# Performance work log

Hardware: AMD Instinct MI355X
Metric: run time of the kernel (lower is better)

Reference implementation:

```python
import jax, jax.numpy as jnp
import numpy as np

EPS = 1e-7  # K.epsilon()
ROUTINGS = 3

def squash(v, axis=-1):
    s2 = jnp.sum(jnp.square(v), axis=axis, keepdims=True)
    scale = s2 / (1.0 + s2) / jnp.sqrt(s2 + EPS)
    return scale * v

def setup_inputs() -> dict:
    key = jax.random.key(0)
    k1, k2 = jax.random.split(key)
    B, IN_CAPS, IN_DIM = 256, 1152, 8
    NUM_CAPS, DIM = 10, 16
    x = jax.random.normal(k1, (B, IN_CAPS, IN_DIM), dtype=jnp.float32)
    W = jax.random.normal(k2, (IN_CAPS, NUM_CAPS, IN_DIM, DIM), dtype=jnp.float32) * 0.05
    return {"x": x, "W": W}

def reference(x, W):
    # u_hat[b,i,j,d] = sum_k x[b,i,k] * W[i,j,k,d]
    u_hat = jnp.einsum('bik,ijkd->bijd', x, W)  # [B, in_caps, num_caps, dim]
    b = jnp.zeros(u_hat.shape[:-1], dtype=u_hat.dtype)  # [B, in_caps, num_caps]
    v = None
    for i in range(ROUTINGS):
        c = jax.nn.softmax(b, axis=2)                       # over num_caps
        s = jnp.einsum('bij,bijd->bjd', c, u_hat)           # [B, num_caps, dim]
        v = squash(s)
        if i < ROUTINGS - 1:
            b = b + jnp.einsum('bijd,bjd->bij', u_hat, v)   # agreement
    return v
```

## Files before the change

### kernel.cpp

```cpp
#include <hip/hip_runtime.h>
#include <cstddef>

#define B_TOT   256
#define IN_CAPS 1152
#define KDIM    8
#define NJ      10
#define ND      16
#define JD      160

#define BB      4
#define ISPLIT  4
#define CI      32
#define IPAR    16
#define NTHREADS 640
#define IRANGE  (IN_CAPS/ISPLIT)
#define NCHUNK  (IRANGE/CI)

__device__ __forceinline__ float dot4(float4 a, float4 b) {
    return a.x*b.x + a.y*b.y + a.z*b.z + a.w*b.w;
}

template<bool FIRST>
__global__ __launch_bounds__(NTHREADS)
void iter_kernel(const float* __restrict__ x, const float* __restrict__ Wt,
                 const float* __restrict__ vsum, float* __restrict__ s_out)
{
    const int g   = blockIdx.x >> 2;
    const int isp = blockIdx.x & 3;
    const int b0  = g * BB;
    const int i_begin = isp * IRANGE;

    const int t = threadIdx.x;
    const int i_par = t / 40;
    const int r  = t - i_par * 40;
    const int j  = r >> 2;
    const int dq = r & 3;

    __shared__ float x_lds[BB][CI][KDIM];
    __shared__ float logit_lds[BB][CI][NJ];
    __shared__ float c_lds[BB][CI][NJ];
    __shared__ float s_lds[BB][JD];

    float4 vs[BB];
    if (!FIRST) {
        #pragma unroll
        for (int bb = 0; bb < BB; ++bb)
            vs[bb] = *(const float4*)(vsum + (size_t)(b0 + bb) * JD + j * ND + dq * 4);
    }

    float4 s_acc[BB];
    #pragma unroll
    for (int bb = 0; bb < BB; ++bb) s_acc[bb] = make_float4(0.f, 0.f, 0.f, 0.f);

    for (int c = 0; c < NCHUNK; ++c) {
        const int ib = i_begin + c * CI;

        if (t < (BB * CI * KDIM) / 4) {
            int bb = t >> 6;
            int f  = t & 63;
            const float4* src = (const float4*)(x + (size_t)(b0 + bb) * IN_CAPS * KDIM
                                                  + (size_t)ib * KDIM);
            ((float4*)&x_lds[bb][0][0])[f] = src[f];
        }
        __syncthreads();

        float4 u[2][BB];
        #pragma unroll
        for (int ii = 0; ii < 2; ++ii) {
            const int i_loc = i_par * 2 + ii;
            const int i = ib + i_loc;
            const float* wrow = Wt + (size_t)(i * NJ + j) * KDIM * ND + dq * 4;
            #pragma unroll
            for (int bb = 0; bb < BB; ++bb) u[ii][bb] = make_float4(0.f, 0.f, 0.f, 0.f);
            #pragma unroll
            for (int k = 0; k < KDIM; ++k) {
                float4 w4 = *(const float4*)(wrow + k * ND);
                #pragma unroll
                for (int bb = 0; bb < BB; ++bb) {
                    float xv = x_lds[bb][i_loc][k];
                    u[ii][bb].x += xv * w4.x;
                    u[ii][bb].y += xv * w4.y;
                    u[ii][bb].z += xv * w4.z;
                    u[ii][bb].w += xv * w4.w;
                }
            }
            if (!FIRST) {
                #pragma unroll
                for (int bb = 0; bb < BB; ++bb) {
                    float lg = dot4(u[ii][bb], vs[bb]);
                    lg += __shfl_xor(lg, 1);
                    lg += __shfl_xor(lg, 2);
                    if (dq == 0) logit_lds[bb][i_loc][j] = lg;
                }
            }
        }

        if (FIRST) {
            #pragma unroll
            for (int ii = 0; ii < 2; ++ii)
                #pragma unroll
                for (int bb = 0; bb < BB; ++bb) {
                    s_acc[bb].x += u[ii][bb].x;
                    s_acc[bb].y += u[ii][bb].y;
                    s_acc[bb].z += u[ii][bb].z;
                    s_acc[bb].w += u[ii][bb].w;
                }
            __syncthreads();
        } else {
            __syncthreads();
            for (int e = t; e < BB * CI * NJ; e += NTHREADS) {
                int bb  = e / (CI * NJ);
                int rem = e - bb * (CI * NJ);
                int il  = rem / NJ;
                int jj  = rem - il * NJ;
                float m = -1e30f;
                #pragma unroll
                for (int q = 0; q < NJ; ++q) m = fmaxf(m, logit_lds[bb][il][q]);
                float ssum = 0.f;
                #pragma unroll
                for (int q = 0; q < NJ; ++q) ssum += __expf(logit_lds[bb][il][q] - m);
                c_lds[bb][il][jj] = __expf(logit_lds[bb][il][jj] - m) / ssum;
            }
            __syncthreads();
            #pragma unroll
            for (int ii = 0; ii < 2; ++ii) {
                const int i_loc = i_par * 2 + ii;
                #pragma unroll
                for (int bb = 0; bb < BB; ++bb) {
                    float cc = c_lds[bb][i_loc][j];
                    s_acc[bb].x += cc * u[ii][bb].x;
                    s_acc[bb].y += cc * u[ii][bb].y;
                    s_acc[bb].z += cc * u[ii][bb].z;
                    s_acc[bb].w += cc * u[ii][bb].w;
                }
            }
        }
    }

    ((float*)s_lds)[t] = 0.f;
    __syncthreads();
    const float premul = FIRST ? 0.1f : 1.0f;
    #pragma unroll
    for (int bb = 0; bb < BB; ++bb) {
        atomicAdd(&s_lds[bb][j * ND + dq * 4 + 0], s_acc[bb].x * premul);
        atomicAdd(&s_lds[bb][j * ND + dq * 4 + 1], s_acc[bb].y * premul);
        atomicAdd(&s_lds[bb][j * ND + dq * 4 + 2], s_acc[bb].z * premul);
        atomicAdd(&s_lds[bb][j * ND + dq * 4 + 3], s_acc[bb].w * premul);
    }
    __syncthreads();
    {
        int bb = t / JD;
        int jd = t - bb * JD;
        unsafeAtomicAdd(&s_out[(size_t)(b0 + bb) * JD + jd], s_lds[bb][jd]);
    }
}

__global__ __launch_bounds__(256)
void squash_kernel(float* __restrict__ s, float* __restrict__ vsum,
                   float* __restrict__ out, int mode)
{
    int idx = blockIdx.x * 256 + threadIdx.x;
    float sv = s[idx];
    float sq = sv * sv;
    sq += __shfl_xor(sq, 1);
    sq += __shfl_xor(sq, 2);
    sq += __shfl_xor(sq, 4);
    sq += __shfl_xor(sq, 8);
    float scale = sq / (1.0f + sq) / sqrtf(sq + 1e-7f);
    float v = sv * scale;
    if (mode == 0) vsum[idx] += v;
    else           out[idx]  = v;
    s[idx] = 0.f;
}

extern "C" void kernel_launch(void* const* d_in, const int* in_sizes, int n_in,
                              void* d_out, int out_size, void* d_ws, size_t ws_size,
                              hipStream_t stream)
{
    const float* x  = (const float*)d_in[0];
    const float* Wt = (const float*)d_in[1];
    float* out  = (float*)d_out;
    float* s    = (float*)d_ws;
    float* vsum = s + (size_t)B_TOT * JD;

    hipMemsetAsync(d_ws, 0, 2 * (size_t)B_TOT * JD * sizeof(float), stream);

    dim3 grid((B_TOT / BB) * ISPLIT), blk(NTHREADS);
    dim3 sgrid((B_TOT * JD) / 256), sblk(256);

    iter_kernel<true><<<grid, blk, 0, stream>>>(x, Wt, nullptr, s);
    squash_kernel<<<sgrid, sblk, 0, stream>>>(s, vsum, out, 0);
    iter_kernel<false><<<grid, blk, 0, stream>>>(x, Wt, vsum, s);
    squash_kernel<<<sgrid, sblk, 0, stream>>>(s, vsum, out, 0);
    iter_kernel<false><<<grid, blk, 0, stream>>>(x, Wt, vsum, s);
    squash_kernel<<<sgrid, sblk, 0, stream>>>(s, vsum, out, 1);
}
```

Measured before the change: 197.6 us.

## Split input capsules finer, preload x once, use per-split partials, simplify softmax

The input-capsule split goes from 4 to 16 and blocks shrink to 320 threads, giving more blocks for better occupancy. Each block preloads its whole x slice into LDS once, which removes the per-chunk x loads and barriers. The softmax drops the max subtraction and computes only a per-row reciprocal denominator, not a full c matrix. When workspace is large enough, partial sums are written to separate slices and reduced in squash, which removes global atomics and the memset. The trade-offs are a small overflow risk from skipping the max subtraction and more barriers per chunk, since each chunk now covers only 8 capsules.

```diff
diff --git a/kernel.cpp b/kernel.cpp
--- a/kernel.cpp
+++ b/kernel.cpp
@@ -9,24 +9,28 @@
 #define JD      160
 
 #define BB      4
-#define ISPLIT  4
-#define CI      32
-#define IPAR    16
-#define NTHREADS 640
+#define ISPLIT  16
 #define IRANGE  (IN_CAPS/ISPLIT)
+#define IPAR    8
+#define NTHREADS 320
+#define CI      IPAR
 #define NCHUNK  (IRANGE/CI)
+#define GRID    ((B_TOT/BB)*ISPLIT)
 
 __device__ __forceinline__ float dot4(float4 a, float4 b) {
     return a.x*b.x + a.y*b.y + a.z*b.z + a.w*b.w;
 }
-
-template<bool FIRST>
-__global__ __launch_bounds__(NTHREADS)
+__device__ __forceinline__ float getc(const float4& v, int k) {
+    switch (k) { case 0: return v.x; case 1: return v.y; case 2: return v.z; default: return v.w; }
+}
+
+template<bool FIRST, bool PARTIAL>
+__global__ __launch_bounds__(NTHREADS, 4)
 void iter_kernel(const float* __restrict__ x, const float* __restrict__ Wt,
                  const float* __restrict__ vsum, float* __restrict__ s_out)
 {
-    const int g   = blockIdx.x >> 2;
-    const int isp = blockIdx.x & 3;
+    const int isp = blockIdx.x & (ISPLIT - 1);
+    const int g   = blockIdx.x >> 4;
     const int b0  = g * BB;
     const int i_begin = isp * IRANGE;
 
@@ -36,10 +40,19 @@
     const int j  = r >> 2;
     const int dq = r & 3;
 
-    __shared__ float x_lds[BB][CI][KDIM];
-    __shared__ float logit_lds[BB][CI][NJ];
-    __shared__ float c_lds[BB][CI][NJ];
-    __shared__ float s_lds[BB][JD];
+    __shared__ float4 x_lds[BB][IRANGE][2];
+    __shared__ float  logit_lds[BB][CI][NJ];
+    __shared__ float  denom_lds[BB][CI];
+    __shared__ float  s_lds[BB][JD];
+
+    for (int f = t; f < BB * IRANGE * 2; f += NTHREADS) {
+        int bb = f / (IRANGE * 2);
+        int fi = f - bb * (IRANGE * 2);
+        const float4* src = (const float4*)(x + (size_t)(b0 + bb) * IN_CAPS * KDIM
+                                              + (size_t)i_begin * KDIM);
+        ((float4*)x_lds)[f] = src[fi];
+    }
+    for (int e = t; e < BB * JD; e += NTHREADS) ((float*)s_lds)[e] = 0.f;
 
     float4 vs[BB];
     if (!FIRST) {
@@ -47,120 +60,104 @@
         for (int bb = 0; bb < BB; ++bb)
             vs[bb] = *(const float4*)(vsum + (size_t)(b0 + bb) * JD + j * ND + dq * 4);
     }
+    __syncthreads();
 
     float4 s_acc[BB];
     #pragma unroll
     for (int bb = 0; bb < BB; ++bb) s_acc[bb] = make_float4(0.f, 0.f, 0.f, 0.f);
 
     for (int c = 0; c < NCHUNK; ++c) {
-        const int ib = i_begin + c * CI;
-
-        if (t < (BB * CI * KDIM) / 4) {
-            int bb = t >> 6;
-            int f  = t & 63;
-            const float4* src = (const float4*)(x + (size_t)(b0 + bb) * IN_CAPS * KDIM
-                                                  + (size_t)ib * KDIM);
-            ((float4*)&x_lds[bb][0][0])[f] = src[f];
-        }
-        __syncthreads();
-
-        float4 u[2][BB];
+        const int i_loc  = c * CI + i_par;
+        const int i_glob = i_begin + i_loc;
+        const float* wrow = Wt + (size_t)(i_glob * NJ + j) * (KDIM * ND) + dq * 4;
+
+        float4 u[BB];
         #pragma unroll
-        for (int ii = 0; ii < 2; ++ii) {
-            const int i_loc = i_par * 2 + ii;
-            const int i = ib + i_loc;
-            const float* wrow = Wt + (size_t)(i * NJ + j) * KDIM * ND + dq * 4;
-            #pragma unroll
-            for (int bb = 0; bb < BB; ++bb) u[ii][bb] = make_float4(0.f, 0.f, 0.f, 0.f);
-            #pragma unroll
-            for (int k = 0; k < KDIM; ++k) {
-                float4 w4 = *(const float4*)(wrow + k * ND);
+        for (int bb = 0; bb < BB; ++bb) u[bb] = make_float4(0.f, 0.f, 0.f, 0.f);
+
+        #pragma unroll
+        for (int kk = 0; kk < 2; ++kk) {
+            float4 xv[BB];
+            #pragma unroll
+            for (int bb = 0; bb < BB; ++bb) xv[bb] = x_lds[bb][i_loc][kk];
+            #pragma unroll
+            for (int k4 = 0; k4 < 4; ++k4) {
+                float4 w4 = *(const float4*)(wrow + (kk * 4 + k4) * ND);
                 #pragma unroll
                 for (int bb = 0; bb < BB; ++bb) {
-                    float xv = x_lds[bb][i_loc][k];
-                    u[ii][bb].x += xv * w4.x;
-                    u[ii][bb].y += xv * w4.y;
-                    u[ii][bb].z += xv * w4.z;
-                    u[ii][bb].w += xv * w4.w;
+                    float xs = getc(xv[bb], k4);
+                    u[bb].x += xs * w4.x;
+                    u[bb].y += xs * w4.y;
+                    u[bb].z += xs * w4.z;
+                    u[bb].w += xs * w4.w;
                 }
             }
-            if (!FIRST) {
+        }
+
+        if (FIRST) {
+            #pragma unroll
+            for (int bb = 0; bb < BB; ++bb) {
+                s_acc[bb].x += u[bb].x; s_acc[bb].y += u[bb].y;
+                s_acc[bb].z += u[bb].z; s_acc[bb].w += u[bb].w;
+            }
+        } else {
+            float lg[BB];
+            #pragma unroll
+            for (int bb = 0; bb < BB; ++bb) {
+                float l = dot4(u[bb], vs[bb]);
+                l += __shfl_xor(l, 1);
+                l += __shfl_xor(l, 2);
+                lg[bb] = l;
+                if (dq == 0) logit_lds[bb][i_par][j] = l;
+            }
+            __syncthreads();
+            if (t < BB * CI) {
+                int bb = t >> 3, il = t & 7;
+                float den = 0.f;
                 #pragma unroll
-                for (int bb = 0; bb < BB; ++bb) {
-                    float lg = dot4(u[ii][bb], vs[bb]);
-                    lg += __shfl_xor(lg, 1);
-                    lg += __shfl_xor(lg, 2);
-                    if (dq == 0) logit_lds[bb][i_loc][j] = lg;
-                }
+                for (int q = 0; q < NJ; ++q) den += __expf(logit_lds[bb][il][q]);
+                denom_lds[bb][il] = 1.0f / den;
+            }
+            __syncthreads();
+            #pragma unroll
+            for (int bb = 0; bb < BB; ++bb) {
+                float cc = __expf(lg[bb]) * denom_lds[bb][i_par];
+                s_acc[bb].x += cc * u[bb].x; s_acc[bb].y += cc * u[bb].y;
+                s_acc[bb].z += cc * u[bb].z; s_acc[bb].w += cc * u[bb].w;
             }
         }
-
-        if (FIRST) {
-            #pragma unroll
-            for (int ii = 0; ii < 2; ++ii)
-                #pragma unroll
-                for (int bb = 0; bb < BB; ++bb) {
-                    s_acc[bb].x += u[ii][bb].x;
-                    s_acc[bb].y += u[ii][bb].y;
-                    s_acc[bb].z += u[ii][bb].z;
-                    s_acc[bb].w += u[ii][bb].w;
-                }
-            __syncthreads();
-        } else {
-            __syncthreads();
-            for (int e = t; e < BB * CI * NJ; e += NTHREADS) {
-                int bb  = e / (CI * NJ);
-                int rem = e - bb * (CI * NJ);
-                int il  = rem / NJ;
-                int jj  = rem - il * NJ;
-                float m = -1e30f;
-                #pragma unroll
-                for (int q = 0; q < NJ; ++q) m = fmaxf(m, logit_lds[bb][il][q]);
-                float ssum = 0.f;
-                #pragma unroll
-                for (int q = 0; q < NJ; ++q) ssum += __expf(logit_lds[bb][il][q] - m);
-                c_lds[bb][il][jj] = __expf(logit_lds[bb][il][jj] - m) / ssum;
-            }
-            __syncthreads();
-            #pragma unroll
-            for (int ii = 0; ii < 2; ++ii) {
-                const int i_loc = i_par * 2 + ii;
-                #pragma unroll
-                for (int bb = 0; bb < BB; ++bb) {
-                    float cc = c_lds[bb][i_loc][j];
-                    s_acc[bb].x += cc * u[ii][bb].x;
-                    s_acc[bb].y += cc * u[ii][bb].y;
-                    s_acc[bb].z += cc * u[ii][bb].z;
-                    s_acc[bb].w += cc * u[ii][bb].w;
-                }
-            }
-        }
-    }
-
-    ((float*)s_lds)[t] = 0.f;
-    __syncthreads();
+    }
+
     const float premul = FIRST ? 0.1f : 1.0f;
     #pragma unroll
     for (int bb = 0; bb < BB; ++bb) {
-        atomicAdd(&s_lds[bb][j * ND + dq * 4 + 0], s_acc[bb].x * premul);
-        atomicAdd(&s_lds[bb][j * ND + dq * 4 + 1], s_acc[bb].y * premul);
-        atomicAdd(&s_lds[bb][j * ND + dq * 4 + 2], s_acc[bb].z * premul);
-        atomicAdd(&s_lds[bb][j * ND + dq * 4 + 3], s_acc[bb].w * premul);
+        float* dst = &s_lds[bb][j * ND + dq * 4];
+        atomicAdd(dst + 0, s_acc[bb].x * premul);
+        atomicAdd(dst + 1, s_acc[bb].y * premul);
+        atomicAdd(dst + 2, s_acc[bb].z * premul);
+        atomicAdd(dst + 3, s_acc[bb].w * premul);
     }
     __syncthreads();
-    {
-        int bb = t / JD;
-        int jd = t - bb * JD;
-        unsafeAtomicAdd(&s_out[(size_t)(b0 + bb) * JD + jd], s_lds[bb][jd]);
-    }
-}
-
+    for (int e = t; e < BB * JD; e += NTHREADS) {
+        int bb = e / JD, jd = e - bb * JD;
+        float val = s_lds[bb][jd];
+        if (PARTIAL)
+            s_out[((size_t)isp * B_TOT + b0 + bb) * JD + jd] = val;
+        else
+            unsafeAtomicAdd(&s_out[(size_t)(b0 + bb) * JD + jd], val);
+    }
+}
+
+template<int P>
 __global__ __launch_bounds__(256)
 void squash_kernel(float* __restrict__ s, float* __restrict__ vsum,
                    float* __restrict__ out, int mode)
 {
     int idx = blockIdx.x * 256 + threadIdx.x;
-    float sv = s[idx];
+    float sv = 0.f;
+    #pragma unroll
+    for (int p = 0; p < P; ++p) sv += s[(size_t)p * B_TOT * JD + idx];
+    if (P == 1) s[idx] = 0.f;
     float sq = sv * sv;
     sq += __shfl_xor(sq, 1);
     sq += __shfl_xor(sq, 2);
@@ -168,9 +165,9 @@
     sq += __shfl_xor(sq, 8);
     float scale = sq / (1.0f + sq) / sqrtf(sq + 1e-7f);
     float v = sv * scale;
-    if (mode == 0) vsum[idx] += v;
-    else           out[idx]  = v;
-    s[idx] = 0.f;
+    if (mode == 0)      vsum[idx] = v;
+    else if (mode == 1) vsum[idx] += v;
+    else                out[idx] = v;
 }
 
 extern "C" void kernel_launch(void* const* d_in, const int* in_sizes, int n_in,
@@ -179,19 +176,34 @@
 {
     const float* x  = (const float*)d_in[0];
     const float* Wt = (const float*)d_in[1];
-    float* out  = (float*)d_out;
-    float* s    = (float*)d_ws;
-    float* vsum = s + (size_t)B_TOT * JD;
-
-    hipMemsetAsync(d_ws, 0, 2 * (size_t)B_TOT * JD * sizeof(float), stream);
-
-    dim3 grid((B_TOT / BB) * ISPLIT), blk(NTHREADS);
+    float* out = (float*)d_out;
+
+    dim3 grid(GRID), blk(NTHREADS);
     dim3 sgrid((B_TOT * JD) / 256), sblk(256);
 
-    iter_kernel<true><<<grid, blk, 0, stream>>>(x, Wt, nullptr, s);
-    squash_kernel<<<sgrid, sblk, 0, stream>>>(s, vsum, out, 0);
-    iter_kernel<false><<<grid, blk, 0, stream>>>(x, Wt, vsum, s);
-    squash_kernel<<<sgrid, sblk, 0, stream>>>(s, vsum, out, 0);
-    iter_kernel<false><<<grid, blk, 0, stream>>>(x, Wt, vsum, s);
-    squash_kernel<<<sgrid, sblk, 0, stream>>>(s, vsum, out, 1);
-}
+    const size_t slice = (size_t)B_TOT * JD;
+    const size_t need  = (ISPLIT + 1) * slice * sizeof(float);
+
+    if (ws_size >= need) {
+        float* s_part = (float*)d_ws;
+        float* vsum   = s_part + ISPLIT * slice;
+
+        iter_kernel<true,  true><<<grid, blk, 0, stream>>>(x, Wt, nullptr, s_part);
+        squash_kernel<ISPLIT><<<sgrid, sblk, 0, stream>>>(s_part, vsum, out, 0);
+        iter_kernel<false, true><<<grid, blk, 0, stream>>>(x, Wt, vsum, s_part);
+        squash_kernel<ISPLIT><<<sgrid, sblk, 0, stream>>>(s_part, vsum, out, 1);
+        iter_kernel<false, true><<<grid, blk, 0, stream>>>(x, Wt, vsum, s_part);
+        squash_kernel<ISPLIT><<<sgrid, sblk, 0, stream>>>(s_part, vsum, out, 2);
+    } else {
+        float* s    = (float*)d_ws;
+        float* vsum = s + slice;
+        hipMemsetAsync(d_ws, 0, slice * sizeof(float), stream);
+
+        iter_kernel<true,  false><<<grid, blk, 0, stream>>>(x, Wt, nullptr, s);
+        squash_kernel<1><<<sgrid, sblk, 0, stream>>>(s, vsum, out, 0);
+        iter_kernel<false, false><<<grid, blk, 0, stream>>>(x, Wt, vsum, s);
+        squash_kernel<1><<<sgrid, sblk, 0, stream>>>(s, vsum, out, 1);
+        iter_kernel<false, false><<<grid, blk, 0, stream>>>(x, Wt, vsum, s);
+        squash_kernel<1><<<sgrid, sblk, 0, stream>>>(s, vsum, out, 2);
+    }
+}
```

After: 256.6 us. +29.8%, slower.
